# Optimization experiments

Hardware: AMD Instinct MI355X
Metric: run time of the kernel (lower is better)

Reference implementation:

```python
import jax, jax.numpy as jnp
import numpy as np

N_NODES = 50000
N_EDGES = 1600000
IN_C, HID_C, OUT_C = 256, 256, 10


def setup_inputs() -> dict:
    key = jax.random.key(0)
    ks = jax.random.split(key, 8)
    x = jax.random.normal(ks[0], (N_NODES, IN_C), dtype=jnp.float32)
    edge_index = jax.random.randint(ks[1], (2, N_EDGES), 0, N_NODES, dtype=jnp.int64)
    s1 = 1.0 / np.sqrt(IN_C)
    s2 = 1.0 / np.sqrt(HID_C)
    W1l = jax.random.normal(ks[2], (IN_C, HID_C), dtype=jnp.float32) * s1
    W1r = jax.random.normal(ks[3], (IN_C, HID_C), dtype=jnp.float32) * s1
    b1 = jnp.zeros((HID_C,), dtype=jnp.float32)
    W2l = jax.random.normal(ks[4], (HID_C, OUT_C), dtype=jnp.float32) * s2
    W2r = jax.random.normal(ks[5], (HID_C, OUT_C), dtype=jnp.float32) * s2
    b2 = jnp.zeros((OUT_C,), dtype=jnp.float32)
    return {"x": x, "edge_index": edge_index, "W1l": W1l, "W1r": W1r,
            "b1": b1, "W2l": W2l, "W2r": W2r, "b2": b2}


def _mean_agg(x, src, dst, n):
    # scatter-mean of source features into destination nodes
    summed = jax.ops.segment_sum(x[src], dst, num_segments=n)  # [N, C]
    cnt = jax.ops.segment_sum(jnp.ones_like(dst, dtype=x.dtype), dst, num_segments=n)
    return summed / jnp.maximum(cnt, 1.0)[:, None]


def _sage_conv(x, src, dst, Wl, Wr, b):
    # PyG SAGEConv (mean aggr): lin_l(mean_j x_j) + lin_r(x_i) + bias
    n = x.shape[0]
    agg = _mean_agg(x, src, dst, n)
    return agg @ Wl + x @ Wr + b


def reference(x, edge_index, W1l, W1r, b1, W2l, W2r, b2):
    src = edge_index[0]
    dst = edge_index[1]
    h = _sage_conv(x, src, dst, W1l, W1r, b1)
    h = jax.nn.relu(h)  # dropout skipped: eval mode
    out = _sage_conv(h, src, dst, W2l, W2r, b2)
    return jax.nn.log_softmax(out, axis=1)
```

## Files before the change

### kernel.cpp

```cpp
#include <hip/hip_runtime.h>
#include <hip/hip_bf16.h>

#define N_NODES 50000
#define N_EDGES 1600000
#define IN_C 256
#define HID_C 256
#define OUT_C 10
#define CD_STRIDE 32
#define SLOT_CAP 96
#define NBUCKET 196
#define EBUF_CAP 9216
#define M_TILES 391
#define PART_BLOCKS 391

typedef short bf16x8 __attribute__((ext_vector_type(8)));
typedef float f32x4 __attribute__((ext_vector_type(4)));

static __device__ __forceinline__ float b2f(short v) {
    unsigned u = (unsigned)(unsigned short)v << 16;
    return __builtin_bit_cast(float, u);
}
static __device__ __forceinline__ short f2b(float f) {
    __hip_bfloat16 h = __float2bfloat16(f);
    return __builtin_bit_cast(short, h);
}
static __device__ __forceinline__ int4 pack8i(float4 a, float4 b) {
    bf16x8 o;
    o[0] = f2b(a.x); o[1] = f2b(a.y); o[2] = f2b(a.z); o[3] = f2b(a.w);
    o[4] = f2b(b.x); o[5] = f2b(b.y); o[6] = f2b(b.z); o[7] = f2b(b.w);
    return __builtin_bit_cast(int4, o);
}

__global__ void k_prep(const float* __restrict__ W1l, const float* __restrict__ W1r,
                       const float* __restrict__ W2l, const float* __restrict__ W2r,
                       __hip_bfloat16* __restrict__ Wt, float* __restrict__ Wt2f) {
    int bid = blockIdx.x;
    if (bid < 512) {
        int idx = bid * 256 + threadIdx.x;
        int n = idx >> 8, k = idx & 255;
        float v = (n < HID_C) ? W1l[k * HID_C + n] : W1r[k * HID_C + (n - HID_C)];
        Wt[idx] = __float2bfloat16(v);
    } else {
        int idx = (bid - 512) * 256 + threadIdx.x;
        int r = idx >> 8, k = idx & 255;
        if (r < OUT_C) Wt2f[r * 256 + k] = W2l[k * OUT_C + r];
        else           Wt2f[(16 + r - OUT_C) * 256 + k] = W2r[k * OUT_C + (r - OUT_C)];
    }
}

__global__ __launch_bounds__(256) void k_gp(
        const int* __restrict__ src, const int* __restrict__ dst,
        int* __restrict__ g_cursor, int* __restrict__ ebuf,
        const float* __restrict__ X, const __hip_bfloat16* __restrict__ Wt,
        const float* __restrict__ b1,
        __hip_bfloat16* __restrict__ Ab, __hip_bfloat16* __restrict__ Bh) {
    __shared__ short Smem[2 * 128 * 64];
    int tid = threadIdx.x;

    if (blockIdx.x < PART_BLOCKS) {
        int* hist = (int*)Smem;
        int* base = hist + 256;
        int* pos  = base + 256;
        if (tid < NBUCKET) { hist[tid] = 0; pos[tid] = 0; }
        __syncthreads();

        int4 s[4], d[4];
        bool valid[4];
#pragma unroll
        for (int q = 0; q < 4; ++q) {
            int idx = blockIdx.x * 1024 + q * 256 + tid;
            valid[q] = (idx < N_EDGES / 4);
            if (valid[q]) {
                s[q] = ((const int4*)src)[idx];
                d[q] = ((const int4*)dst)[idx];
            }
        }
#pragma unroll
        for (int q = 0; q < 4; ++q) {
            if (valid[q]) {
                atomicAdd(&hist[d[q].x >> 8], 1);
                atomicAdd(&hist[d[q].y >> 8], 1);
                atomicAdd(&hist[d[q].z >> 8], 1);
                atomicAdd(&hist[d[q].w >> 8], 1);
            }
        }
        __syncthreads();
        if (tid < NBUCKET && hist[tid] > 0)
            base[tid] = atomicAdd(&g_cursor[tid], hist[tid]);
        __syncthreads();
#pragma unroll
        for (int q = 0; q < 4; ++q) {
            if (valid[q]) {
                int ss[4] = { s[q].x, s[q].y, s[q].z, s[q].w };
                int dd[4] = { d[q].x, d[q].y, d[q].z, d[q].w };
#pragma unroll
                for (int e = 0; e < 4; ++e) {
                    int b = dd[e] >> 8;
                    int p = base[b] + atomicAdd(&pos[b], 1);
                    if (p < EBUF_CAP)
                        ebuf[b * EBUF_CAP + p] = ss[e] | ((dd[e] & 255) << 16);
                }
            }
        }
        return;
    }

    short* As = Smem;
    short* Bs = Smem + 128 * 64;
    int fid = blockIdx.x - PART_BLOCKS;
    int xcd = fid & 7, slot = fid >> 3;
    int m_t = (slot >> 2) * 8 + xcd;
    if (m_t >= M_TILES) return;
    int n_t = slot & 3;
    int m_base = m_t * 128;
    int n_base = n_t * 128;

    int wave = tid >> 6, lane = tid & 63;
    int r = lane & 15, quad = lane >> 4;
    int wr = wave >> 1, wc = wave & 1;

    int srow = tid >> 3;
    int kb8  = (tid & 7) * 16;
    int kelem = (tid & 7) * 8;
    int swz  = kb8 ^ ((srow & 7) << 4);

    f32x4 acc[4][4];
#pragma unroll
    for (int i = 0; i < 4; ++i)
#pragma unroll
        for (int j = 0; j < 4; ++j) acc[i][j] = f32x4{0.f, 0.f, 0.f, 0.f};

    int4 av[4], bv[4];
#pragma unroll
    for (int q = 0; q < 4; ++q) {
        int grow = m_base + q * 32 + srow;
        if (grow > N_NODES - 1) grow = N_NODES - 1;
        const float* xp = X + (size_t)grow * IN_C + kelem;
        av[q] = pack8i(*(const float4*)xp, *(const float4*)(xp + 4));
        int brow = n_base + q * 32 + srow;
        bv[q] = *(const int4*)((const char*)Wt + ((size_t)brow * 512 + kb8));
    }

    for (int kk = 0; kk < 4; ++kk) {
        if (kk) __syncthreads();
#pragma unroll
        for (int q = 0; q < 4; ++q) {
            *(int4*)((char*)As + (size_t)((q * 32 + srow) * 128 + swz)) = av[q];
            *(int4*)((char*)Bs + (size_t)((q * 32 + srow) * 128 + swz)) = bv[q];
        }
        __syncthreads();

        if (kk < 3) {
            int ke = (kk + 1) * 64 + kelem;
            int kbyte = (kk + 1) * 128 + kb8;
#pragma unroll
            for (int q = 0; q < 4; ++q) {
                int grow = m_base + q * 32 + srow;
                if (grow > N_NODES - 1) grow = N_NODES - 1;
                const float* xp = X + (size_t)grow * IN_C + ke;
                av[q] = pack8i(*(const float4*)xp, *(const float4*)(xp + 4));
                int brow = n_base + q * 32 + srow;
                bv[q] = *(const int4*)((const char*)Wt + ((size_t)brow * 512 + kbyte));
            }
        }

#pragma unroll
        for (int s = 0; s < 2; ++s) {
            int kfb = (s * 64 + quad * 16) ^ ((r & 7) << 4);
            bf16x8 a[4], b[4];
#pragma unroll
            for (int i = 0; i < 4; ++i)
                a[i] = *(const bf16x8*)((const char*)As + (size_t)((wr * 64 + i * 16 + r) * 128) + kfb);
#pragma unroll
            for (int j = 0; j < 4; ++j)
                b[j] = *(const bf16x8*)((const char*)Bs + (size_t)((wc * 64 + j * 16 + r) * 128) + kfb);
#pragma unroll
            for (int i = 0; i < 4; ++i)
#pragma unroll
                for (int j = 0; j < 4; ++j)
                    acc[i][j] = __builtin_amdgcn_mfma_f32_16x16x32_bf16(a[i], b[j], acc[i][j], 0, 0, 0);
        }
    }

    __syncthreads();
    short* Cs = Smem;
    bool left = (n_base < HID_C);
#pragma unroll
    for (int j = 0; j < 4; ++j) {
        int coll = wc * 64 + 16 * j + r;
        float bias = left ? 0.f : b1[n_base + coll - HID_C];
#pragma unroll
        for (int i = 0; i < 4; ++i) {
#pragma unroll
            for (int ii = 0; ii < 4; ++ii) {
                int rowl = wr * 64 + 16 * i + quad * 4 + ii;
                int byteoff = (coll * 2) ^ ((rowl & 7) << 4);
                *(short*)((char*)Cs + rowl * 256 + byteoff) = f2b(acc[i][j][ii] + bias);
            }
        }
    }
    __syncthreads();

    int rrow = tid >> 4;
    int cchunk = (tid & 15) * 16;
    size_t colbyte = left ? (size_t)(n_base * 2) : (size_t)((n_base - HID_C) * 2);
    char* outp = left ? (char*)Ab : (char*)Bh;
    for (int rb = 0; rb < 128; rb += 16) {
        int rowl = rb + rrow;
        int4 v = *(const int4*)((const char*)Cs + rowl * 256 + (cchunk ^ ((rowl & 7) << 4)));
        int grow = m_base + rowl;
        if (grow < N_NODES)
            *(int4*)(outp + (size_t)grow * 512 + colbyte + cchunk) = v;
    }
}

__global__ __launch_bounds__(512) void k_bucket(const int* __restrict__ ebuf,
                                                const int* __restrict__ g_cursor,
                                                int* __restrict__ cnt,
                                                unsigned short* __restrict__ slots) {
    __shared__ int lcnt[256];
    int b = blockIdx.x, tid = threadIdx.x;
    if (tid < 256) lcnt[tid] = 0;
    __syncthreads();
    int n_e = g_cursor[b];
    if (n_e > EBUF_CAP) n_e = EBUF_CAP;
    const int* eb = ebuf + b * EBUF_CAP;
    int n4 = n_e >> 2;
    for (int t = tid; t < n4; t += 512) {
        int4 v = ((const int4*)eb)[t];
        int vv[4] = { v.x, v.y, v.z, v.w };
#pragma unroll
        for (int e = 0; e < 4; ++e) {
            int dl = (vv[e] >> 16) & 255;
            int sv = vv[e] & 0xFFFF;
            int p = atomicAdd(&lcnt[dl], 1);
            if (p < SLOT_CAP) slots[(size_t)(b * 256 + dl) * SLOT_CAP + p] = (unsigned short)sv;
        }
    }
    for (int t = (n4 << 2) + tid; t < n_e; t += 512) {
        int vv = eb[t];
        int dl = (vv >> 16) & 255;
        int sv = vv & 0xFFFF;
        int p = atomicAdd(&lcnt[dl], 1);
        if (p < SLOT_CAP) slots[(size_t)(b * 256 + dl) * SLOT_CAP + p] = (unsigned short)sv;
    }
    __syncthreads();
    if (tid < 256) {
        int nid = b * 256 + tid;
        if (nid < N_NODES) cnt[nid] = lcnt[tid];
    }
}

__global__ __launch_bounds__(256) void k_agg1f(
        const __hip_bfloat16* __restrict__ Ab, const __hip_bfloat16* __restrict__ Bh,
        const int* __restrict__ cnt, const unsigned short* __restrict__ slots,
        const float* __restrict__ Wt2f, const float* __restrict__ b2,
        float* __restrict__ CD) {
    int wave = threadIdx.x >> 6, lane = threadIdx.x & 63;
    int nid = blockIdx.x * 4 + wave;
    int half = lane >> 5;
    int c8 = (lane & 31) * 8;
    const unsigned short* row = slots + (size_t)nid * SLOT_CAP;
    int n = cnt[nid];
    if (n > SLOT_CAP) n = SLOT_CAP;
    int mid = (n + 1) >> 1;
    int beg = half ? mid : 0;
    int end = half ? n : mid;

    float s0[8], s1[8], s2[8], s3[8];
#pragma unroll
    for (int j = 0; j < 8; ++j) { s0[j] = 0.f; s1[j] = 0.f; s2[j] = 0.f; s3[j] = 0.f; }

    const __hip_bfloat16* abc = Ab + c8;
    int e = beg;
    for (; e + 4 <= end; e += 4) {
        int i0 = row[e], i1 = row[e + 1], i2 = row[e + 2], i3 = row[e + 3];
        bf16x8 v0 = *(const bf16x8*)(abc + (size_t)i0 * HID_C);
        bf16x8 v1 = *(const bf16x8*)(abc + (size_t)i1 * HID_C);
        bf16x8 v2 = *(const bf16x8*)(abc + (size_t)i2 * HID_C);
        bf16x8 v3 = *(const bf16x8*)(abc + (size_t)i3 * HID_C);
#pragma unroll
        for (int j = 0; j < 8; ++j) {
            s0[j] += b2f(v0[j]); s1[j] += b2f(v1[j]);
            s2[j] += b2f(v2[j]); s3[j] += b2f(v3[j]);
        }
    }
    for (; e < end; ++e) {
        int i0 = row[e];
        bf16x8 v0 = *(const bf16x8*)(abc + (size_t)i0 * HID_C);
#pragma unroll
        for (int j = 0; j < 8; ++j) s0[j] += b2f(v0[j]);
    }
#pragma unroll
    for (int j = 0; j < 8; ++j) s0[j] += (s1[j] + s2[j]) + s3[j];
#pragma unroll
    for (int j = 0; j < 8; ++j) s0[j] += __shfl_down(s0[j], 32, 64);

    float h[8];
    float inv = 1.f / fmaxf((float)n, 1.f);
    if (half == 0) {
        bf16x8 bb = *(const bf16x8*)(Bh + (size_t)nid * HID_C + c8);
#pragma unroll
        for (int j = 0; j < 8; ++j)
            h[j] = fmaxf(s0[j] * inv + b2f(bb[j]), 0.f);
    }
#pragma unroll
    for (int j = 0; j < 8; ++j) h[j] = __shfl(h[j], lane & 31, 64);

    const float* wbase = Wt2f + (half ? 16 * 256 : 0);
    float acc[10];
#pragma unroll
    for (int j = 0; j < 10; ++j) {
        f32x4 w0 = *(const f32x4*)(wbase + j * 256 + c8);
        f32x4 w1 = *(const f32x4*)(wbase + j * 256 + c8 + 4);
        float a = h[0] * w0[0] + h[1] * w0[1] + h[2] * w0[2] + h[3] * w0[3]
                + h[4] * w1[0] + h[5] * w1[1] + h[6] * w1[2] + h[7] * w1[3];
#pragma unroll
        for (int off = 16; off > 0; off >>= 1)
            a += __shfl_down(a, off, 32);
        acc[j] = a;
    }
    if ((lane & 31) == 0) {
        float* o = CD + (size_t)nid * CD_STRIDE + half * 16;
        if (half == 0) {
#pragma unroll
            for (int j = 0; j < 10; ++j) o[j] = acc[j];
            o[10] = 0.f; o[11] = 0.f;
        } else {
#pragma unroll
            for (int j = 0; j < 10; ++j) o[j] = acc[j] + b2[j];
        }
    }
}

__global__ __launch_bounds__(256) void k_agg2(
        const float* __restrict__ CD, const int* __restrict__ cnt,
        const unsigned short* __restrict__ slots, float* __restrict__ out) {
    int wave = threadIdx.x >> 6, lane = threadIdx.x & 63;
    int half = lane >> 5, sub = lane & 31;
    int nid = blockIdx.x * 8 + wave * 2 + half;
    const unsigned short* row = slots + (size_t)nid * SLOT_CAP;
    int n = cnt[nid];
    if (n > SLOT_CAP) n = SLOT_CAP;
    float s[10];
#pragma unroll
    for (int j = 0; j < 10; ++j) s[j] = 0.f;
    for (int e = sub; e < n; e += 32) {
        const float* cr = CD + (size_t)row[e] * CD_STRIDE;
        f32x4 v0 = *(const f32x4*)cr;
        f32x4 v1 = *(const f32x4*)(cr + 4);
        f32x4 v2 = *(const f32x4*)(cr + 8);
#pragma unroll
        for (int j = 0; j < 4; ++j) { s[j] += v0[j]; s[4 + j] += v1[j]; }
        s[8] += v2[0]; s[9] += v2[1];
    }
#pragma unroll
    for (int j = 0; j < 10; ++j)
#pragma unroll
        for (int off = 16; off > 0; off >>= 1)
            s[j] += __shfl_down(s[j], off, 32);
    if (sub == 0) {
        float inv = 1.f / fmaxf((float)n, 1.f);
        float z[10], mx = -1e30f;
#pragma unroll
        for (int j = 0; j < 10; ++j) {
            z[j] = s[j] * inv + CD[(size_t)nid * CD_STRIDE + 16 + j];
            mx = fmaxf(mx, z[j]);
        }
        float se = 0.f;
#pragma unroll
        for (int j = 0; j < 10; ++j) se += expf(z[j] - mx);
        float lse = logf(se) + mx;
#pragma unroll
        for (int j = 0; j < 10; ++j) out[(size_t)nid * OUT_C + j] = z[j] - lse;
    }
}

extern "C" void kernel_launch(void* const* d_in, const int* in_sizes, int n_in,
                              void* d_out, int out_size, void* d_ws, size_t ws_size,
                              hipStream_t stream) {
    const float* x   = (const float*)d_in[0];
    const int*   ei  = (const int*)d_in[1];
    const float* W1l = (const float*)d_in[2];
    const float* W1r = (const float*)d_in[3];
    const float* b1  = (const float*)d_in[4];
    const float* W2l = (const float*)d_in[5];
    const float* W2r = (const float*)d_in[6];
    const float* b2  = (const float*)d_in[7];
    float* out = (float*)d_out;
    const int* src = ei;
    const int* dst = ei + N_EDGES;

    char* w = (char*)d_ws;
    size_t off = 0;
    auto alloc = [&](size_t bytes) -> void* {
        void* p = w + off;
        off = (off + bytes + 255) & ~(size_t)255;
        return p;
    };
    __hip_bfloat16* Wt   = (__hip_bfloat16*)alloc((size_t)2 * HID_C * IN_C * 2);
    float*          Wt2f = (float*)alloc((size_t)32 * 256 * 4);
    __hip_bfloat16* Ab   = (__hip_bfloat16*)alloc((size_t)N_NODES * HID_C * 2);
    __hip_bfloat16* Bh   = (__hip_bfloat16*)alloc((size_t)N_NODES * HID_C * 2);
    float* CD = (float*)alloc((size_t)N_NODES * CD_STRIDE * 4);
    int* cnt      = (int*)alloc((size_t)N_NODES * 4);
    unsigned short* slots = (unsigned short*)alloc((size_t)N_NODES * SLOT_CAP * 2);
    int* g_cursor = (int*)alloc((size_t)NBUCKET * 4);
    int* ebuf     = (int*)alloc((size_t)NBUCKET * EBUF_CAP * 4);

    (void)hipMemsetAsync(g_cursor, 0, (size_t)NBUCKET * 4, stream);

    k_prep<<<532, 256, 0, stream>>>(W1l, W1r, W2l, W2r, Wt, Wt2f);
    k_gp<<<PART_BLOCKS + 8 * 196, 256, 0, stream>>>(src, dst, g_cursor, ebuf,
                                                    x, Wt, b1, Ab, Bh);
    k_bucket<<<NBUCKET, 512, 0, stream>>>(ebuf, g_cursor, cnt, slots);
    k_agg1f<<<N_NODES / 4, 256, 0, stream>>>(Ab, Bh, cnt, slots, Wt2f, b2, CD);
    k_agg2<<<N_NODES / 8, 256, 0, stream>>>(CD, cnt, slots, out);
}
```

Baseline: 316.0 us.

## Regroup kernels: partition with weight prep, bucketing with GEMM; split CD arrays

Moves the edge-partition pass into the weight-prep kernel and the per-bucket slot fill into the layer-1 GEMM kernel, so the five launches become four. Each bucket pass now overlaps the GEMM tiles instead of running as its own serial kernel. The second-layer scratch is split into two compact 12-float arrays (left and right halves) instead of one 32-float stride, which cuts the bytes fetched per neighbour gather in the final aggregation. Bucket blocks drop from 512 to 256 threads, so each bucket does more serial work and may finish later.

Result: no change. 313.3 us, median of 2 (-0.8%).

```diff
diff --git a/kernel.cpp b/kernel.cpp
--- a/kernel.cpp
+++ b/kernel.cpp
@@ -6,12 +6,12 @@
 #define IN_C 256
 #define HID_C 256
 #define OUT_C 10
-#define CD_STRIDE 32
 #define SLOT_CAP 96
 #define NBUCKET 196
 #define EBUF_CAP 9216
 #define M_TILES 391
 #define PART_BLOCKS 391
+#define PREP_BLOCKS 532
 
 typedef short bf16x8 __attribute__((ext_vector_type(8)));
 typedef float f32x4 __attribute__((ext_vector_type(4)));
@@ -31,83 +31,123 @@
     return __builtin_bit_cast(int4, o);
 }
 
-__global__ void k_prep(const float* __restrict__ W1l, const float* __restrict__ W1r,
-                       const float* __restrict__ W2l, const float* __restrict__ W2r,
-                       __hip_bfloat16* __restrict__ Wt, float* __restrict__ Wt2f) {
+__global__ __launch_bounds__(256) void k_pp(
+        const float* __restrict__ W1l, const float* __restrict__ W1r,
+        const float* __restrict__ W2l, const float* __restrict__ W2r,
+        __hip_bfloat16* __restrict__ Wt, float* __restrict__ Wt2f,
+        const int* __restrict__ src, const int* __restrict__ dst,
+        int* __restrict__ g_cursor, int* __restrict__ ebuf) {
+    __shared__ int pbuf[3 * 256];
+    int tid = threadIdx.x;
     int bid = blockIdx.x;
+
     if (bid < 512) {
-        int idx = bid * 256 + threadIdx.x;
+        int idx = bid * 256 + tid;
         int n = idx >> 8, k = idx & 255;
         float v = (n < HID_C) ? W1l[k * HID_C + n] : W1r[k * HID_C + (n - HID_C)];
         Wt[idx] = __float2bfloat16(v);
-    } else {
-        int idx = (bid - 512) * 256 + threadIdx.x;
+        return;
+    }
+    if (bid < PREP_BLOCKS) {
+        int idx = (bid - 512) * 256 + tid;
         int r = idx >> 8, k = idx & 255;
         if (r < OUT_C) Wt2f[r * 256 + k] = W2l[k * OUT_C + r];
         else           Wt2f[(16 + r - OUT_C) * 256 + k] = W2r[k * OUT_C + (r - OUT_C)];
-    }
-}
-
-__global__ __launch_bounds__(256) void k_gp(
-        const int* __restrict__ src, const int* __restrict__ dst,
-        int* __restrict__ g_cursor, int* __restrict__ ebuf,
+        return;
+    }
+
+    int* hist = pbuf;
+    int* base = pbuf + 256;
+    int* pos  = pbuf + 512;
+    int pb = bid - PREP_BLOCKS;
+    if (tid < NBUCKET) { hist[tid] = 0; pos[tid] = 0; }
+    __syncthreads();
+
+    int4 s[4], d[4];
+    bool valid[4];
+#pragma unroll
+    for (int q = 0; q < 4; ++q) {
+        int idx = pb * 1024 + q * 256 + tid;
+        valid[q] = (idx < N_EDGES / 4);
+        if (valid[q]) {
+            s[q] = ((const int4*)src)[idx];
+            d[q] = ((const int4*)dst)[idx];
+        }
+    }
+#pragma unroll
+    for (int q = 0; q < 4; ++q) {
+        if (valid[q]) {
+            atomicAdd(&hist[d[q].x >> 8], 1);
+            atomicAdd(&hist[d[q].y >> 8], 1);
+            atomicAdd(&hist[d[q].z >> 8], 1);
+            atomicAdd(&hist[d[q].w >> 8], 1);
+        }
+    }
+    __syncthreads();
+    if (tid < NBUCKET && hist[tid] > 0)
+        base[tid] = atomicAdd(&g_cursor[tid], hist[tid]);
+    __syncthreads();
+#pragma unroll
+    for (int q = 0; q < 4; ++q) {
+        if (valid[q]) {
+            int ss[4] = { s[q].x, s[q].y, s[q].z, s[q].w };
+            int dd[4] = { d[q].x, d[q].y, d[q].z, d[q].w };
+#pragma unroll
+            for (int e = 0; e < 4; ++e) {
+                int b = dd[e] >> 8;
+                int p = base[b] + atomicAdd(&pos[b], 1);
+                if (p < EBUF_CAP)
+                    ebuf[b * EBUF_CAP + p] = ss[e] | ((dd[e] & 255) << 16);
+            }
+        }
+    }
+}
+
+__global__ __launch_bounds__(256) void k_gb(
+        const int* __restrict__ ebuf, const int* __restrict__ g_cursor,
+        int* __restrict__ cnt, unsigned short* __restrict__ slots,
         const float* __restrict__ X, const __hip_bfloat16* __restrict__ Wt,
         const float* __restrict__ b1,
         __hip_bfloat16* __restrict__ Ab, __hip_bfloat16* __restrict__ Bh) {
     __shared__ short Smem[2 * 128 * 64];
     int tid = threadIdx.x;
 
-    if (blockIdx.x < PART_BLOCKS) {
-        int* hist = (int*)Smem;
-        int* base = hist + 256;
-        int* pos  = base + 256;
-        if (tid < NBUCKET) { hist[tid] = 0; pos[tid] = 0; }
+    if (blockIdx.x < NBUCKET) {
+        int* lcnt = (int*)Smem;
+        int b = blockIdx.x;
+        lcnt[tid] = 0;
         __syncthreads();
-
-        int4 s[4], d[4];
-        bool valid[4];
-#pragma unroll
-        for (int q = 0; q < 4; ++q) {
-            int idx = blockIdx.x * 1024 + q * 256 + tid;
-            valid[q] = (idx < N_EDGES / 4);
-            if (valid[q]) {
-                s[q] = ((const int4*)src)[idx];
-                d[q] = ((const int4*)dst)[idx];
+        int n_e = g_cursor[b];
+        if (n_e > EBUF_CAP) n_e = EBUF_CAP;
+        const int* eb = ebuf + b * EBUF_CAP;
+        int n4 = n_e >> 2;
+        for (int t = tid; t < n4; t += 256) {
+            int4 v = ((const int4*)eb)[t];
+            int vv[4] = { v.x, v.y, v.z, v.w };
+#pragma unroll
+            for (int e = 0; e < 4; ++e) {
+                int dl = (vv[e] >> 16) & 255;
+                int sv = vv[e] & 0xFFFF;
+                int p = atomicAdd(&lcnt[dl], 1);
+                if (p < SLOT_CAP) slots[(size_t)(b * 256 + dl) * SLOT_CAP + p] = (unsigned short)sv;
             }
         }
-#pragma unroll
-        for (int q = 0; q < 4; ++q) {
-            if (valid[q]) {
-                atomicAdd(&hist[d[q].x >> 8], 1);
-                atomicAdd(&hist[d[q].y >> 8], 1);
-                atomicAdd(&hist[d[q].z >> 8], 1);
-                atomicAdd(&hist[d[q].w >> 8], 1);
-            }
+        for (int t = (n4 << 2) + tid; t < n_e; t += 256) {
+            int vv = eb[t];
+            int dl = (vv >> 16) & 255;
+            int sv = vv & 0xFFFF;
+            int p = atomicAdd(&lcnt[dl], 1);
+            if (p < SLOT_CAP) slots[(size_t)(b * 256 + dl) * SLOT_CAP + p] = (unsigned short)sv;
         }
         __syncthreads();
-        if (tid < NBUCKET && hist[tid] > 0)
-            base[tid] = atomicAdd(&g_cursor[tid], hist[tid]);
-        __syncthreads();
-#pragma unroll
-        for (int q = 0; q < 4; ++q) {
-            if (valid[q]) {
-                int ss[4] = { s[q].x, s[q].y, s[q].z, s[q].w };
-                int dd[4] = { d[q].x, d[q].y, d[q].z, d[q].w };
-#pragma unroll
-                for (int e = 0; e < 4; ++e) {
-                    int b = dd[e] >> 8;
-                    int p = base[b] + atomicAdd(&pos[b], 1);
-                    if (p < EBUF_CAP)
-                        ebuf[b * EBUF_CAP + p] = ss[e] | ((dd[e] & 255) << 16);
-                }
-            }
-        }
+        int nid = b * 256 + tid;
+        if (nid < N_NODES) cnt[nid] = lcnt[tid];
         return;
     }
 
     short* As = Smem;
     short* Bs = Smem + 128 * 64;
-    int fid = blockIdx.x - PART_BLOCKS;
+    int fid = blockIdx.x - NBUCKET;
     int xcd = fid & 7, slot = fid >> 3;
     int m_t = (slot >> 2) * 8 + xcd;
     if (m_t >= M_TILES) return;
@@ -214,48 +254,11 @@
     }
 }
 
-__global__ __launch_bounds__(512) void k_bucket(const int* __restrict__ ebuf,
-                                                const int* __restrict__ g_cursor,
-                                                int* __restrict__ cnt,
-                                                unsigned short* __restrict__ slots) {
-    __shared__ int lcnt[256];
-    int b = blockIdx.x, tid = threadIdx.x;
-    if (tid < 256) lcnt[tid] = 0;
-    __syncthreads();
-    int n_e = g_cursor[b];
-    if (n_e > EBUF_CAP) n_e = EBUF_CAP;
-    const int* eb = ebuf + b * EBUF_CAP;
-    int n4 = n_e >> 2;
-    for (int t = tid; t < n4; t += 512) {
-        int4 v = ((const int4*)eb)[t];
-        int vv[4] = { v.x, v.y, v.z, v.w };
-#pragma unroll
-        for (int e = 0; e < 4; ++e) {
-            int dl = (vv[e] >> 16) & 255;
-            int sv = vv[e] & 0xFFFF;
-            int p = atomicAdd(&lcnt[dl], 1);
-            if (p < SLOT_CAP) slots[(size_t)(b * 256 + dl) * SLOT_CAP + p] = (unsigned short)sv;
-        }
-    }
-    for (int t = (n4 << 2) + tid; t < n_e; t += 512) {
-        int vv = eb[t];
-        int dl = (vv >> 16) & 255;
-        int sv = vv & 0xFFFF;
-        int p = atomicAdd(&lcnt[dl], 1);
-        if (p < SLOT_CAP) slots[(size_t)(b * 256 + dl) * SLOT_CAP + p] = (unsigned short)sv;
-    }
-    __syncthreads();
-    if (tid < 256) {
-        int nid = b * 256 + tid;
-        if (nid < N_NODES) cnt[nid] = lcnt[tid];
-    }
-}
-
 __global__ __launch_bounds__(256) void k_agg1f(
         const __hip_bfloat16* __restrict__ Ab, const __hip_bfloat16* __restrict__ Bh,
         const int* __restrict__ cnt, const unsigned short* __restrict__ slots,
         const float* __restrict__ Wt2f, const float* __restrict__ b2,
-        float* __restrict__ CD) {
+        float* __restrict__ CDl, float* __restrict__ CDr) {
     int wave = threadIdx.x >> 6, lane = threadIdx.x & 63;
     int nid = blockIdx.x * 4 + wave;
     int half = lane >> 5;
@@ -321,12 +324,13 @@
         acc[j] = a;
     }
     if ((lane & 31) == 0) {
-        float* o = CD + (size_t)nid * CD_STRIDE + half * 16;
         if (half == 0) {
+            float* o = CDl + (size_t)nid * 12;
 #pragma unroll
             for (int j = 0; j < 10; ++j) o[j] = acc[j];
             o[10] = 0.f; o[11] = 0.f;
         } else {
+            float* o = CDr + (size_t)nid * 12;
 #pragma unroll
             for (int j = 0; j < 10; ++j) o[j] = acc[j] + b2[j];
         }
@@ -334,8 +338,9 @@
 }
 
 __global__ __launch_bounds__(256) void k_agg2(
-        const float* __restrict__ CD, const int* __restrict__ cnt,
-        const unsigned short* __restrict__ slots, float* __restrict__ out) {
+        const float* __restrict__ CDl, const float* __restrict__ CDr,
+        const int* __restrict__ cnt, const unsigned short* __restrict__ slots,
+        float* __restrict__ out) {
     int wave = threadIdx.x >> 6, lane = threadIdx.x & 63;
     int half = lane >> 5, sub = lane & 31;
     int nid = blockIdx.x * 8 + wave * 2 + half;
@@ -346,7 +351,7 @@
 #pragma unroll
     for (int j = 0; j < 10; ++j) s[j] = 0.f;
     for (int e = sub; e < n; e += 32) {
-        const float* cr = CD + (size_t)row[e] * CD_STRIDE;
+        const float* cr = CDl + (size_t)row[e] * 12;
         f32x4 v0 = *(const f32x4*)cr;
         f32x4 v1 = *(const f32x4*)(cr + 4);
         f32x4 v2 = *(const f32x4*)(cr + 8);
@@ -361,10 +366,11 @@
             s[j] += __shfl_down(s[j], off, 32);
     if (sub == 0) {
         float inv = 1.f / fmaxf((float)n, 1.f);
+        const float* rr = CDr + (size_t)nid * 12;
         float z[10], mx = -1e30f;
 #pragma unroll
         for (int j = 0; j < 10; ++j) {
-            z[j] = s[j] * inv + CD[(size_t)nid * CD_STRIDE + 16 + j];
+            z[j] = s[j] * inv + rr[j];
             mx = fmaxf(mx, z[j]);
         }
         float se = 0.f;
@@ -402,7 +408,8 @@
     float*          Wt2f = (float*)alloc((size_t)32 * 256 * 4);
     __hip_bfloat16* Ab   = (__hip_bfloat16*)alloc((size_t)N_NODES * HID_C * 2);
     __hip_bfloat16* Bh   = (__hip_bfloat16*)alloc((size_t)N_NODES * HID_C * 2);
-    float* CD = (float*)alloc((size_t)N_NODES * CD_STRIDE * 4);
+    float* CDl = (float*)alloc((size_t)N_NODES * 12 * 4);
+    float* CDr = (float*)alloc((size_t)N_NODES * 12 * 4);
     int* cnt      = (int*)alloc((size_t)N_NODES * 4);
     unsigned short* slots = (unsigned short*)alloc((size_t)N_NODES * SLOT_CAP * 2);
     int* g_cursor = (int*)alloc((size_t)NBUCKET * 4);
@@ -410,10 +417,10 @@
 
     (void)hipMemsetAsync(g_cursor, 0, (size_t)NBUCKET * 4, stream);
 
-    k_prep<<<532, 256, 0, stream>>>(W1l, W1r, W2l, W2r, Wt, Wt2f);
-    k_gp<<<PART_BLOCKS + 8 * 196, 256, 0, stream>>>(src, dst, g_cursor, ebuf,
-                                                    x, Wt, b1, Ab, Bh);
-    k_bucket<<<NBUCKET, 512, 0, stream>>>(ebuf, g_cursor, cnt, slots);
-    k_agg1f<<<N_NODES / 4, 256, 0, stream>>>(Ab, Bh, cnt, slots, Wt2f, b2, CD);
-    k_agg2<<<N_NODES / 8, 256, 0, stream>>>(CD, cnt, slots, out);
-}
+    k_pp<<<PREP_BLOCKS + PART_BLOCKS, 256, 0, stream>>>(W1l, W1r, W2l, W2r, Wt, Wt2f,
+                                                        src, dst, g_cursor, ebuf);
+    k_gb<<<NBUCKET + 8 * 196, 256, 0, stream>>>(ebuf, g_cursor, cnt, slots,
+                                                x, Wt, b1, Ab, Bh);
+    k_agg1f<<<N_NODES / 4, 256, 0, stream>>>(Ab, Bh, cnt, slots, Wt2f, b2, CDl, CDr);
+    k_agg2<<<N_NODES / 8, 256, 0, stream>>>(CDl, CDr, cnt, slots, out);
+}
```
